# Optimization experiments

Measured on AMD Instinct MI355X. Metric: run time of the kernel, lower is better.

The kernel has to match this reference:

```python
import jax, jax.numpy as jnp
import numpy as np

B, H, M, N, D = 8, 8, 512, 512, 64
HID = 16
MIX1 = (1.0 / 2.0) ** 0.5
MIX2 = (1.0 / 16.0) ** 0.5


def setup_inputs() -> dict:
    key = jax.random.key(0)
    ks = jax.random.split(key, 8)
    q = jax.random.normal(ks[0], (B, H, M, D), dtype=jnp.float32)
    k = jax.random.normal(ks[1], (B, H, N, D), dtype=jnp.float32)
    v = jax.random.normal(ks[2], (B, H, N, D), dtype=jnp.float32)
    dmat = jax.random.uniform(ks[3], (B, M, N), dtype=jnp.float32)
    mix_W1 = jax.random.uniform(ks[4], (H, 2, HID), minval=-MIX1, maxval=MIX1, dtype=jnp.float32)
    mix_b1 = jax.random.uniform(ks[5], (H, HID), minval=-MIX1, maxval=MIX1, dtype=jnp.float32)
    mix_W2 = jax.random.uniform(ks[6], (H, HID, 1), minval=-MIX2, maxval=MIX2, dtype=jnp.float32)
    mix_b2 = jax.random.uniform(ks[7], (H, 1), minval=-MIX2, maxval=MIX2, dtype=jnp.float32)
    return {"q": q, "k": k, "v": v, "dmat": dmat,
            "mix_W1": mix_W1, "mix_b1": mix_b1, "mix_W2": mix_W2, "mix_b2": mix_b2}


def reference(q, k, v, dmat, mix_W1, mix_b1, mix_W2, mix_b2):
    # attention scores: [b,h,m,n]
    scale = 1.0 / jnp.sqrt(jnp.float32(k.shape[-1]))
    scores = jnp.einsum("bhmd,bhnd->bhmn", q, k) * scale
    # stack dot-product scores with distance matrix: [b,h,m,n,2]
    mixed = jnp.stack([scores, jnp.broadcast_to(dmat[:, None, :, :], scores.shape)], axis=-1)
    # per-head 2-layer MLP over the 2-channel axis
    h1 = jax.nn.relu(jnp.einsum("bhmnc,hcf->bhmnf", mixed, mix_W1)
                     + mix_b1[None, :, None, None, :])          # [b,h,m,n,HID]
    mixed_scores = (jnp.einsum("bhmnf,hfo->bhmno", h1, mix_W2)[..., 0]
                    + mix_b2[None, :, None, None, 0])            # [b,h,m,n]
    attn = jax.nn.softmax(mixed_scores, axis=-1)
    return jnp.einsum("bhmn,bhnd->bhmd", attn, v)
```

## Files before the change

kernel.cpp:

```cpp
#include <hip/hip_runtime.h>
#include <hip/hip_bf16.h>


typedef __attribute__((ext_vector_type(4))) float f32x4;
typedef __attribute__((ext_vector_type(8))) __bf16 bf16x8;
typedef __attribute__((ext_vector_type(4))) unsigned short us4;
typedef __attribute__((ext_vector_type(8))) unsigned short us8;

union U8 { us8 u; bf16x8 b; };

static __device__ __forceinline__ unsigned short bf_hi(float x) {
    unsigned int u = __float_as_uint(x);
    u += 0x7fffu + ((u >> 16) & 1u);
    return (unsigned short)(u >> 16);
}
static __device__ __forceinline__ float bf_f(unsigned short s) {
    return __uint_as_float(((unsigned int)s) << 16);
}
static __device__ __forceinline__ float rlf(float x) {
    return __uint_as_float(__builtin_amdgcn_readfirstlane(__float_as_uint(x)));
}

static __device__ __forceinline__ int sw64(int row, int col) {
    return row * 64 + ((((col >> 3) ^ (row & 7)) << 3) | (col & 7));
}
static __device__ __forceinline__ int swdm(int row, int col) {
    return row * 64 + ((((col >> 2) ^ (row & 15)) << 2) | (col & 3));
}

#define B_ 8
#define H_ 8
#define M_ 512
#define N_ 512
#define D_ 64
#define HID_ 16

__global__ __launch_bounds__(256, 2) void msdpa_kernel(
    const float* __restrict__ qg, const float* __restrict__ kg,
    const float* __restrict__ vg, const float* __restrict__ dg,
    const float* __restrict__ w1g, const float* __restrict__ b1g,
    const float* __restrict__ w2g, float* __restrict__ outg)
{
    extern __shared__ f32x4 smem4[];
    unsigned short* KH  = (unsigned short*)smem4;
    unsigned short* KL  = KH + 4096;
    unsigned short* VTH = KL + 4096;
    unsigned short* VTL = VTH + 4096;
    float*          DM  = (float*)(VTL + 4096);
    unsigned short* PH  = (unsigned short*)(DM + 4096);
    unsigned short* PL  = PH + 4096;

    const int tid  = threadIdx.x;
    const int lane = tid & 63;
    const int wv   = tid >> 6;
    const int r16  = lane & 15;
    const int g    = lane >> 4;

    const int bm = blockIdx.x;
    const int h  = blockIdx.y;
    const int b  = blockIdx.z;

    unsigned short* PHw = PH + wv * 1024;
    unsigned short* PLw = PL + wv * 1024;

    const float* w1h = w1g + h * 2 * HID_;
    const float* b1h = b1g + h * HID_;
    const float* w2h = w2g + h * HID_;
    float ap[HID_], cc[HID_], bb[HID_], wp[HID_];
#pragma unroll
    for (int f = 0; f < HID_; ++f) {
        ap[f] = rlf(w1h[f]) * 0.125f;
        cc[f] = rlf(w1h[HID_ + f]);
        bb[f] = rlf(b1h[f]);
        wp[f] = rlf(w2h[f]) * 1.4426950408889634f;
    }

    const long bh = (long)(b * H_ + h);
    const float* qbase = qg + (bh * M_ + (long)bm * 64 + wv * 16 + r16) * D_;
    bf16x8 qh[2], ql[2];
#pragma unroll
    for (int ks = 0; ks < 2; ++ks) {
        f32x4 x0 = *(const f32x4*)(qbase + ks * 32 + g * 8);
        f32x4 x1 = *(const f32x4*)(qbase + ks * 32 + g * 8 + 4);
        U8 uh, ul;
#pragma unroll
        for (int j = 0; j < 8; ++j) {
            float xv = (j < 4) ? x0[j] : x1[j - 4];
            unsigned short hs = bf_hi(xv);
            uh.u[j] = hs;
            ul.u[j] = bf_hi(xv - bf_f(hs));
        }
        qh[ks] = uh.b; ql[ks] = ul.b;
    }

    f32x4 oacc[4];
#pragma unroll
    for (int dt = 0; dt < 4; ++dt) oacc[dt] = f32x4{0.f, 0.f, 0.f, 0.f};
    float mrun = -1e30f, lsum = 0.0f;

    const float* kbase = kg + bh * N_ * D_;
    const float* vbase = vg + bh * N_ * D_;
    const float* dbase = dg + ((long)b * M_ + (long)bm * 64) * N_;

    for (int nt = 0; nt < 8; ++nt) {
        const int n0 = nt * 64;
        __syncthreads();
#pragma unroll
        for (int it = 0; it < 4; ++it) {
            int e  = it * 1024 + tid * 4;
            int rr = e >> 6, c0 = e & 63;
            f32x4 kk = *(const f32x4*)(kbase + (long)(n0 + rr) * D_ + c0);
            us4 khs, kls;
#pragma unroll
            for (int i = 0; i < 4; ++i) {
                unsigned short hs = bf_hi(kk[i]);
                khs[i] = hs; kls[i] = bf_hi(kk[i] - bf_f(hs));
            }
            int kidx = sw64(rr, c0);
            *(us4*)(KH + kidx) = khs;
            *(us4*)(KL + kidx) = kls;
            f32x4 vv = *(const f32x4*)(vbase + (long)(n0 + rr) * D_ + c0);
#pragma unroll
            for (int i = 0; i < 4; ++i) {
                unsigned short hs = bf_hi(vv[i]);
                VTH[sw64(c0 + i, rr)] = hs;
                VTL[sw64(c0 + i, rr)] = bf_hi(vv[i] - bf_f(hs));
            }
            f32x4 dd = *(const f32x4*)(dbase + (long)rr * N_ + n0 + c0);
            *(f32x4*)(DM + swdm(rr, c0)) = dd;
        }
        __syncthreads();

        f32x4 sacc[4];
#pragma unroll
        for (int n16 = 0; n16 < 4; ++n16) sacc[n16] = f32x4{0.f, 0.f, 0.f, 0.f};
#pragma unroll
        for (int n16 = 0; n16 < 4; ++n16) {
            int row = n16 * 16 + r16;
#pragma unroll
            for (int ks = 0; ks < 2; ++ks) {
                int off = sw64(row, ks * 32 + g * 8);
                bf16x8 kh_ = *(bf16x8*)(KH + off);
                bf16x8 kl_ = *(bf16x8*)(KL + off);
                sacc[n16] = __builtin_amdgcn_mfma_f32_16x16x32_bf16(kh_, qh[ks], sacc[n16], 0, 0, 0);
                sacc[n16] = __builtin_amdgcn_mfma_f32_16x16x32_bf16(kh_, ql[ks], sacc[n16], 0, 0, 0);
                sacc[n16] = __builtin_amdgcn_mfma_f32_16x16x32_bf16(kl_, qh[ks], sacc[n16], 0, 0, 0);
            }
        }

        const int dmrow = wv * 16 + r16;
        f32x4 dmv[4];
#pragma unroll
        for (int n16 = 0; n16 < 4; ++n16)
            dmv[n16] = *(const f32x4*)(DM + swdm(dmrow, n16 * 16 + g * 4));
        float ms[4][4];
#pragma unroll
        for (int n16 = 0; n16 < 4; ++n16)
#pragma unroll
            for (int r = 0; r < 4; ++r) ms[n16][r] = 0.0f;
#pragma unroll
        for (int f = 0; f < HID_; ++f) {
            float a = ap[f], c = cc[f], bcst = bb[f], w = wp[f];
#pragma unroll
            for (int n16 = 0; n16 < 4; ++n16)
#pragma unroll
                for (int r = 0; r < 4; ++r) {
                    float u = fmaf(a, sacc[n16][r], fmaf(c, dmv[n16][r], bcst));
                    ms[n16][r] = fmaf(w, fmaxf(u, 0.0f), ms[n16][r]);
                }
        }

        float mloc = -1e30f;
#pragma unroll
        for (int n16 = 0; n16 < 4; ++n16)
#pragma unroll
            for (int r = 0; r < 4; ++r) mloc = fmaxf(mloc, ms[n16][r]);
        mloc = fmaxf(mloc, __shfl_xor(mloc, 16));
        mloc = fmaxf(mloc, __shfl_xor(mloc, 32));
        float mnew = fmaxf(mrun, mloc);
        float sc = exp2f(mrun - mnew);
        mrun = mnew;

        float psum = 0.0f;
#pragma unroll
        for (int n16 = 0; n16 < 4; ++n16) {
            us4 phs, pls;
#pragma unroll
            for (int r = 0; r < 4; ++r) {
                float p = exp2f(ms[n16][r] - mnew);
                psum += p;
                unsigned short hs = bf_hi(p);
                phs[r] = hs;
                pls[r] = bf_hi(p - bf_f(hs));
            }
            int pidx = sw64(r16, n16 * 16 + g * 4);
            *(us4*)(PHw + pidx) = phs;
            *(us4*)(PLw + pidx) = pls;
        }
        lsum = lsum * sc + psum;

        float scm[4];
#pragma unroll
        for (int r = 0; r < 4; ++r) scm[r] = __shfl(sc, g * 4 + r);
#pragma unroll
        for (int dt = 0; dt < 4; ++dt)
#pragma unroll
            for (int r = 0; r < 4; ++r) oacc[dt][r] *= scm[r];

#pragma unroll
        for (int ks = 0; ks < 2; ++ks) {
            int poff = sw64(r16, ks * 32 + g * 8);
            bf16x8 pa = *(bf16x8*)(PHw + poff);
            bf16x8 pb = *(bf16x8*)(PLw + poff);
#pragma unroll
            for (int dt = 0; dt < 4; ++dt) {
                int voff = sw64(dt * 16 + r16, ks * 32 + g * 8);
                bf16x8 vh_ = *(bf16x8*)(VTH + voff);
                bf16x8 vl_ = *(bf16x8*)(VTL + voff);
                oacc[dt] = __builtin_amdgcn_mfma_f32_16x16x32_bf16(pa, vh_, oacc[dt], 0, 0, 0);
                oacc[dt] = __builtin_amdgcn_mfma_f32_16x16x32_bf16(pa, vl_, oacc[dt], 0, 0, 0);
                oacc[dt] = __builtin_amdgcn_mfma_f32_16x16x32_bf16(pb, vh_, oacc[dt], 0, 0, 0);
            }
        }
    }

    lsum += __shfl_xor(lsum, 16);
    lsum += __shfl_xor(lsum, 32);
    float linv[4];
#pragma unroll
    for (int r = 0; r < 4; ++r) linv[r] = 1.0f / __shfl(lsum, g * 4 + r);

    float* obase = outg + (bh * M_ + (long)bm * 64 + wv * 16) * D_;
#pragma unroll
    for (int dt = 0; dt < 4; ++dt)
#pragma unroll
        for (int r = 0; r < 4; ++r)
            obase[(g * 4 + r) * D_ + dt * 16 + r16] = oacc[dt][r] * linv[r];
}

extern "C" void kernel_launch(void* const* d_in, const int* in_sizes, int n_in,
                              void* d_out, int out_size, void* d_ws, size_t ws_size,
                              hipStream_t stream) {
    const float* q  = (const float*)d_in[0];
    const float* k  = (const float*)d_in[1];
    const float* v  = (const float*)d_in[2];
    const float* dm = (const float*)d_in[3];
    const float* w1 = (const float*)d_in[4];
    const float* b1 = (const float*)d_in[5];
    const float* w2 = (const float*)d_in[6];
    float* out = (float*)d_out;

    (void)hipFuncSetAttribute(reinterpret_cast<const void*>(msdpa_kernel),
                              hipFuncAttributeMaxDynamicSharedMemorySize, 65536);
    dim3 grid(M_ / 64, H_, B_);
    msdpa_kernel<<<grid, dim3(256), 65536, stream>>>(q, k, v, dm, w1, b1, w2, out);
}
```

Before: 156.1 us.

## Precompute split-bf16 K/V tiles in a prep kernel and DMA them to LDS

A new prep kernel converts K and transposed V once per (b,h) into hi/lo bf16 tiles in workspace, already swizzled. The main kernel then copies those tiles into LDS with global_load_lds, so the 8 M-blocks no longer each redo the conversion and transpose. The distance matrix is read straight from global memory instead of being staged through LDS. The MLP is rewritten using relu(u)=(u+|u|)/2, which folds the linear half into precomputed constants. The cost is an extra launch plus a workspace write and read.

Result: faster. 132.6 us (-15.0%).

```diff
diff --git a/kernel.cpp b/kernel.cpp
--- a/kernel.cpp
+++ b/kernel.cpp
@@ -4,28 +4,22 @@
 
 typedef __attribute__((ext_vector_type(4))) float f32x4;
 typedef __attribute__((ext_vector_type(8))) __bf16 bf16x8;
-typedef __attribute__((ext_vector_type(4))) unsigned short us4;
-typedef __attribute__((ext_vector_type(8))) unsigned short us8;
-
-union U8 { us8 u; bf16x8 b; };
-
-static __device__ __forceinline__ unsigned short bf_hi(float x) {
-    unsigned int u = __float_as_uint(x);
-    u += 0x7fffu + ((u >> 16) & 1u);
-    return (unsigned short)(u >> 16);
-}
-static __device__ __forceinline__ float bf_f(unsigned short s) {
-    return __uint_as_float(((unsigned int)s) << 16);
-}
+typedef __attribute__((ext_vector_type(4))) __bf16 bf16x4;
+
 static __device__ __forceinline__ float rlf(float x) {
     return __uint_as_float(__builtin_amdgcn_readfirstlane(__float_as_uint(x)));
 }
-
+static __device__ __forceinline__ void cvt2(float x, __bf16& h, __bf16& l) {
+    h = (__bf16)x;
+    l = (__bf16)(x - (float)h);
+}
 static __device__ __forceinline__ int sw64(int row, int col) {
     return row * 64 + ((((col >> 3) ^ (row & 7)) << 3) | (col & 7));
 }
-static __device__ __forceinline__ int swdm(int row, int col) {
-    return row * 64 + ((((col >> 2) ^ (row & 15)) << 2) | (col & 3));
+static __device__ __forceinline__ void dma16(const __bf16* g, __bf16* l) {
+    __builtin_amdgcn_global_load_lds(
+        (const __attribute__((address_space(1))) unsigned*)g,
+        (__attribute__((address_space(3))) unsigned*)l, 16, 0, 0);
 }
 
 #define B_ 8
@@ -35,20 +29,70 @@
 #define D_ 64
 #define HID_ 16
 
+__global__ __launch_bounds__(256) void prep_kernel(
+    const float* __restrict__ kg, const float* __restrict__ vg,
+    __bf16* __restrict__ ws)
+{
+    __shared__ float vld[64 * 68];
+    const int t   = threadIdx.x;
+    const int blk = blockIdx.x;
+    const long base = (long)blk * 4096;
+    __bf16* out = ws + (long)blk * 16384;
+
+#pragma unroll
+    for (int it = 0; it < 4; ++it) {
+        const int e = it * 1024 + t * 4;
+        const int rr = e >> 6, c0 = e & 63;
+        f32x4 v4 = *(const f32x4*)(vg + base + e);
+        *(f32x4*)(vld + rr * 68 + c0) = v4;
+    }
+
+#pragma unroll
+    for (int qq = t; qq < 512; qq += 256) {
+        const int row = qq >> 3, c = qq & 7;
+        const float* src = kg + base + row * 64 + ((c ^ (row & 7)) << 3);
+        f32x4 a = *(const f32x4*)src;
+        f32x4 b4 = *(const f32x4*)(src + 4);
+        bf16x8 hv, lv;
+#pragma unroll
+        for (int j = 0; j < 4; ++j) {
+            __bf16 h, l;
+            cvt2(a[j], h, l);  hv[j] = h;     lv[j] = l;
+            cvt2(b4[j], h, l); hv[4 + j] = h; lv[4 + j] = l;
+        }
+        *(bf16x8*)(out + qq * 8) = hv;
+        *(bf16x8*)(out + 4096 + qq * 8) = lv;
+    }
+    __syncthreads();
+
+#pragma unroll
+    for (int qq = t; qq < 512; qq += 256) {
+        const int d = qq & 63, c = qq >> 6;
+        bf16x8 hv, lv;
+#pragma unroll
+        for (int j = 0; j < 8; ++j) {
+            const int n = ((c ^ (d & 7)) << 3) + j;
+            __bf16 h, l;
+            cvt2(vld[n * 68 + d], h, l);
+            hv[j] = h; lv[j] = l;
+        }
+        const int pos = d * 64 + c * 8;
+        *(bf16x8*)(out + 8192 + pos) = hv;
+        *(bf16x8*)(out + 12288 + pos) = lv;
+    }
+}
+
 __global__ __launch_bounds__(256, 2) void msdpa_kernel(
-    const float* __restrict__ qg, const float* __restrict__ kg,
-    const float* __restrict__ vg, const float* __restrict__ dg,
-    const float* __restrict__ w1g, const float* __restrict__ b1g,
-    const float* __restrict__ w2g, float* __restrict__ outg)
+    const float* __restrict__ qg, const __bf16* __restrict__ ws,
+    const float* __restrict__ dg, const float* __restrict__ w1g,
+    const float* __restrict__ b1g, const float* __restrict__ w2g,
+    float* __restrict__ outg)
 {
-    extern __shared__ f32x4 smem4[];
-    unsigned short* KH  = (unsigned short*)smem4;
-    unsigned short* KL  = KH + 4096;
-    unsigned short* VTH = KL + 4096;
-    unsigned short* VTL = VTH + 4096;
-    float*          DM  = (float*)(VTL + 4096);
-    unsigned short* PH  = (unsigned short*)(DM + 4096);
-    unsigned short* PL  = PH + 4096;
+    extern __shared__ __bf16 smem[];
+    __bf16* KH  = smem;
+    __bf16* KL  = smem + 4096;
+    __bf16* VTH = smem + 8192;
+    __bf16* VTL = smem + 12288;
 
     const int tid  = threadIdx.x;
     const int lane = tid & 63;
@@ -60,19 +104,23 @@
     const int h  = blockIdx.y;
     const int b  = blockIdx.z;
 
-    unsigned short* PHw = PH + wv * 1024;
-    unsigned short* PLw = PL + wv * 1024;
+    __bf16* PHw = smem + 16384 + wv * 1024;
+    __bf16* PLw = smem + 20480 + wv * 1024;
 
     const float* w1h = w1g + h * 2 * HID_;
     const float* b1h = b1g + h * HID_;
     const float* w2h = w2g + h * HID_;
-    float ap[HID_], cc[HID_], bb[HID_], wp[HID_];
+    float af[HID_], cf[HID_], bf_[HID_], wa[HID_];
+    float A = 0.f, C = 0.f, B0 = 0.f;
 #pragma unroll
     for (int f = 0; f < HID_; ++f) {
-        ap[f] = rlf(w1h[f]) * 0.125f;
-        cc[f] = rlf(w1h[HID_ + f]);
-        bb[f] = rlf(b1h[f]);
-        wp[f] = rlf(w2h[f]) * 1.4426950408889634f;
+        af[f] = rlf(w1h[f]) * 0.125f;
+        cf[f] = rlf(w1h[HID_ + f]);
+        bf_[f] = rlf(b1h[f]);
+        wa[f] = rlf(w2h[f]) * (1.4426950408889634f * 0.5f);
+        A  = fmaf(wa[f], af[f], A);
+        C  = fmaf(wa[f], cf[f], C);
+        B0 = fmaf(wa[f], bf_[f], B0);
     }
 
     const long bh = (long)(b * H_ + h);
@@ -82,15 +130,14 @@
     for (int ks = 0; ks < 2; ++ks) {
         f32x4 x0 = *(const f32x4*)(qbase + ks * 32 + g * 8);
         f32x4 x1 = *(const f32x4*)(qbase + ks * 32 + g * 8 + 4);
-        U8 uh, ul;
-#pragma unroll
-        for (int j = 0; j < 8; ++j) {
-            float xv = (j < 4) ? x0[j] : x1[j - 4];
-            unsigned short hs = bf_hi(xv);
-            uh.u[j] = hs;
-            ul.u[j] = bf_hi(xv - bf_f(hs));
-        }
-        qh[ks] = uh.b; ql[ks] = ul.b;
+        bf16x8 hv, lv;
+#pragma unroll
+        for (int j = 0; j < 4; ++j) {
+            __bf16 h_, l_;
+            cvt2(x0[j], h_, l_); hv[j] = h_; lv[j] = l_;
+            cvt2(x1[j], h_, l_); hv[4 + j] = h_; lv[4 + j] = l_;
+        }
+        qh[ks] = hv; ql[ks] = lv;
     }
 
     f32x4 oacc[4];
@@ -98,77 +145,53 @@
     for (int dt = 0; dt < 4; ++dt) oacc[dt] = f32x4{0.f, 0.f, 0.f, 0.f};
     float mrun = -1e30f, lsum = 0.0f;
 
-    const float* kbase = kg + bh * N_ * D_;
-    const float* vbase = vg + bh * N_ * D_;
-    const float* dbase = dg + ((long)b * M_ + (long)bm * 64) * N_;
+    const __bf16* wsbh = ws + bh * (8L * 16384);
+    const float* dmp = dg + ((long)b * M_ + (long)bm * 64 + wv * 16 + r16) * N_ + g * 4;
 
     for (int nt = 0; nt < 8; ++nt) {
-        const int n0 = nt * 64;
         __syncthreads();
-#pragma unroll
-        for (int it = 0; it < 4; ++it) {
-            int e  = it * 1024 + tid * 4;
-            int rr = e >> 6, c0 = e & 63;
-            f32x4 kk = *(const f32x4*)(kbase + (long)(n0 + rr) * D_ + c0);
-            us4 khs, kls;
-#pragma unroll
-            for (int i = 0; i < 4; ++i) {
-                unsigned short hs = bf_hi(kk[i]);
-                khs[i] = hs; kls[i] = bf_hi(kk[i] - bf_f(hs));
-            }
-            int kidx = sw64(rr, c0);
-            *(us4*)(KH + kidx) = khs;
-            *(us4*)(KL + kidx) = kls;
-            f32x4 vv = *(const f32x4*)(vbase + (long)(n0 + rr) * D_ + c0);
-#pragma unroll
-            for (int i = 0; i < 4; ++i) {
-                unsigned short hs = bf_hi(vv[i]);
-                VTH[sw64(c0 + i, rr)] = hs;
-                VTL[sw64(c0 + i, rr)] = bf_hi(vv[i] - bf_f(hs));
-            }
-            f32x4 dd = *(const f32x4*)(dbase + (long)rr * N_ + n0 + c0);
-            *(f32x4*)(DM + swdm(rr, c0)) = dd;
-        }
+        const __bf16* tile = wsbh + nt * 16384;
+#pragma unroll
+        for (int i = 0; i < 8; ++i)
+            dma16(tile + i * 2048 + tid * 8, smem + i * 2048 + tid * 8);
         __syncthreads();
 
+        f32x4 dmv[4];
+#pragma unroll
+        for (int n16 = 0; n16 < 4; ++n16)
+            dmv[n16] = *(const f32x4*)(dmp + nt * 64 + n16 * 16);
+
         f32x4 sacc[4];
 #pragma unroll
         for (int n16 = 0; n16 < 4; ++n16) sacc[n16] = f32x4{0.f, 0.f, 0.f, 0.f};
 #pragma unroll
         for (int n16 = 0; n16 < 4; ++n16) {
-            int row = n16 * 16 + r16;
+            const int row = n16 * 16 + r16;
 #pragma unroll
             for (int ks = 0; ks < 2; ++ks) {
-                int off = sw64(row, ks * 32 + g * 8);
-                bf16x8 kh_ = *(bf16x8*)(KH + off);
-                bf16x8 kl_ = *(bf16x8*)(KL + off);
+                const int off = sw64(row, ks * 32 + g * 8);
+                bf16x8 kh_ = *(const bf16x8*)(KH + off);
+                bf16x8 kl_ = *(const bf16x8*)(KL + off);
                 sacc[n16] = __builtin_amdgcn_mfma_f32_16x16x32_bf16(kh_, qh[ks], sacc[n16], 0, 0, 0);
                 sacc[n16] = __builtin_amdgcn_mfma_f32_16x16x32_bf16(kh_, ql[ks], sacc[n16], 0, 0, 0);
                 sacc[n16] = __builtin_amdgcn_mfma_f32_16x16x32_bf16(kl_, qh[ks], sacc[n16], 0, 0, 0);
             }
         }
 
-        const int dmrow = wv * 16 + r16;
-        f32x4 dmv[4];
+        float ms[4][4];
 #pragma unroll
         for (int n16 = 0; n16 < 4; ++n16)
-            dmv[n16] = *(const f32x4*)(DM + swdm(dmrow, n16 * 16 + g * 4));
-        float ms[4][4];
-#pragma unroll
-        for (int n16 = 0; n16 < 4; ++n16)
-#pragma unroll
-            for (int r = 0; r < 4; ++r) ms[n16][r] = 0.0f;
-#pragma unroll
-        for (int f = 0; f < HID_; ++f) {
-            float a = ap[f], c = cc[f], bcst = bb[f], w = wp[f];
-#pragma unroll
-            for (int n16 = 0; n16 < 4; ++n16)
-#pragma unroll
-                for (int r = 0; r < 4; ++r) {
-                    float u = fmaf(a, sacc[n16][r], fmaf(c, dmv[n16][r], bcst));
-                    ms[n16][r] = fmaf(w, fmaxf(u, 0.0f), ms[n16][r]);
+#pragma unroll
+            for (int r = 0; r < 4; ++r) {
+                const float s = sacc[n16][r], d = dmv[n16][r];
+                float acc = fmaf(A, s, fmaf(C, d, B0));
+#pragma unroll
+                for (int f = 0; f < HID_; ++f) {
+                    const float u = fmaf(af[f], s, fmaf(cf[f], d, bf_[f]));
+                    acc = fmaf(wa[f], fabsf(u), acc);
                 }
-        }
+                ms[n16][r] = acc;
+            }
 
         float mloc = -1e30f;
 #pragma unroll
@@ -177,25 +200,26 @@
             for (int r = 0; r < 4; ++r) mloc = fmaxf(mloc, ms[n16][r]);
         mloc = fmaxf(mloc, __shfl_xor(mloc, 16));
         mloc = fmaxf(mloc, __shfl_xor(mloc, 32));
-        float mnew = fmaxf(mrun, mloc);
-        float sc = exp2f(mrun - mnew);
+        const float mnew = fmaxf(mrun, mloc);
+        const float sc = exp2f(mrun - mnew);
         mrun = mnew;
 
         float psum = 0.0f;
 #pragma unroll
         for (int n16 = 0; n16 < 4; ++n16) {
-            us4 phs, pls;
+            bf16x4 ph4, pl4;
 #pragma unroll
             for (int r = 0; r < 4; ++r) {
-                float p = exp2f(ms[n16][r] - mnew);
+                const float p = exp2f(ms[n16][r] - mnew);
                 psum += p;
-                unsigned short hs = bf_hi(p);
-                phs[r] = hs;
-                pls[r] = bf_hi(p - bf_f(hs));
-            }
-            int pidx = sw64(r16, n16 * 16 + g * 4);
-            *(us4*)(PHw + pidx) = phs;
-            *(us4*)(PLw + pidx) = pls;
+                __bf16 h_, l_;
+                cvt2(p, h_, l_);
+                ph4[r] = h_; pl4[r] = l_;
+            }
+            const int cc = 2 * n16 + (g >> 1);
+            const int pos = r16 * 64 + (((cc ^ (r16 & 7)) << 3) | ((g & 1) << 2));
+            *(bf16x4*)(PHw + pos) = ph4;
+            *(bf16x4*)(PLw + pos) = pl4;
         }
         lsum = lsum * sc + psum;
 
@@ -209,17 +233,17 @@
 
 #pragma unroll
         for (int ks = 0; ks < 2; ++ks) {
-            int poff = sw64(r16, ks * 32 + g * 8);
-            bf16x8 pa = *(bf16x8*)(PHw + poff);
-            bf16x8 pb = *(bf16x8*)(PLw + poff);
+            const int pofs = r16 * 64 + ((((ks * 4 + g)) ^ (r16 & 7)) << 3);
+            bf16x8 pa = *(const bf16x8*)(PHw + pofs);
+            bf16x8 pb = *(const bf16x8*)(PLw + pofs);
 #pragma unroll
             for (int dt = 0; dt < 4; ++dt) {
-                int voff = sw64(dt * 16 + r16, ks * 32 + g * 8);
-                bf16x8 vh_ = *(bf16x8*)(VTH + voff);
-                bf16x8 vl_ = *(bf16x8*)(VTL + voff);
-                oacc[dt] = __builtin_amdgcn_mfma_f32_16x16x32_bf16(pa, vh_, oacc[dt], 0, 0, 0);
-                oacc[dt] = __builtin_amdgcn_mfma_f32_16x16x32_bf16(pa, vl_, oacc[dt], 0, 0, 0);
-                oacc[dt] = __builtin_amdgcn_mfma_f32_16x16x32_bf16(pb, vh_, oacc[dt], 0, 0, 0);
+                const int vofs = sw64(dt * 16 + r16, ks * 32 + g * 8);
+                bf16x8 vh = *(const bf16x8*)(VTH + vofs);
+                bf16x8 vl = *(const bf16x8*)(VTL + vofs);
+                oacc[dt] = __builtin_amdgcn_mfma_f32_16x16x32_bf16(pa, vh, oacc[dt], 0, 0, 0);
+                oacc[dt] = __builtin_amdgcn_mfma_f32_16x16x32_bf16(pa, vl, oacc[dt], 0, 0, 0);
+                oacc[dt] = __builtin_amdgcn_mfma_f32_16x16x32_bf16(pb, vh, oacc[dt], 0, 0, 0);
             }
         }
     }
@@ -249,9 +273,12 @@
     const float* b1 = (const float*)d_in[5];
     const float* w2 = (const float*)d_in[6];
     float* out = (float*)d_out;
+    __bf16* ws = (__bf16*)d_ws;
+
+    prep_kernel<<<dim3(512), dim3(256), 0, stream>>>(k, v, ws);
 
     (void)hipFuncSetAttribute(reinterpret_cast<const void*>(msdpa_kernel),
                               hipFuncAttributeMaxDynamicSharedMemorySize, 65536);
     dim3 grid(M_ / 64, H_, B_);
-    msdpa_kernel<<<grid, dim3(256), 65536, stream>>>(q, k, v, dm, w1, b1, w2, out);
-}
+    msdpa_kernel<<<grid, dim3(256), 49152, stream>>>(q, ws, dm, w1, b1, w2, out);
+}
```
